# Kernel optimization log

Measured on AMD Instinct MI355X. Metric: run time of the kernel, lower is better.

Reference implementation:

```python
import jax, jax.numpy as jnp
import numpy as np

D_MODEL = 1024
N_HEADS = 16
D_K = 64
BATCH = 2
SEQ = 2048
LN_EPS = 1e-5


def setup_inputs() -> dict:
    key = jax.random.key(0)
    ks = jax.random.split(key, 6)
    s = 1.0 / np.sqrt(D_MODEL)
    return {
        "h": jax.random.normal(ks[0], (BATCH, SEQ, D_MODEL), dtype=jnp.float32),
        "Wq": jax.random.normal(ks[1], (D_MODEL, D_MODEL), dtype=jnp.float32) * s,
        "bq": jnp.zeros((D_MODEL,), jnp.float32),
        "Wk": jax.random.normal(ks[2], (D_MODEL, D_MODEL), dtype=jnp.float32) * s,
        "bk": jnp.zeros((D_MODEL,), jnp.float32),
        "Wv": jax.random.normal(ks[3], (D_MODEL, D_MODEL), dtype=jnp.float32) * s,
        "bv": jnp.zeros((D_MODEL,), jnp.float32),
        "Wo": jax.random.normal(ks[4], (D_MODEL, D_MODEL), dtype=jnp.float32) * s,
        "bo": jnp.zeros((D_MODEL,), jnp.float32),
        "ln_w": jnp.ones((D_MODEL,), jnp.float32),
        "ln_b": jnp.zeros((D_MODEL,), jnp.float32),
    }


def _layernorm(x, w, b):
    mu = jnp.mean(x, axis=-1, keepdims=True)
    var = jnp.var(x, axis=-1, keepdims=True)
    return (x - mu) * jax.lax.rsqrt(var + LN_EPS) * w + b


def reference(h, Wq, bq, Wk, bk, Wv, bv, Wo, bo, ln_w, ln_b):
    b, s, _ = h.shape
    scale = 1.0 / np.sqrt(D_K)
    h_res = h
    hn = _layernorm(h, ln_w, ln_b)
    # Linear layers (torch convention: y = x @ W.T + b), split into heads
    q = (hn @ Wq.T + bq).reshape(b, s, N_HEADS, D_K)
    k = (hn @ Wk.T + bk).reshape(b, s, N_HEADS, D_K)
    v = (hn @ Wv.T + bv).reshape(b, s, N_HEADS, D_K)
    attn = jnp.einsum('bihd,bjhd->bhij', q, k) * scale  # [b, h, i, j]
    attn = jax.nn.softmax(attn, axis=-1)
    o = jnp.einsum('bhij,bjhd->bihd', attn, v).reshape(b, s, N_HEADS * D_K)
    out = o @ Wo.T + bo
    return out + h_res
```

## Files before the change

kernel.cpp:

```cpp
#include <hip/hip_runtime.h>
#include <cstdint>

#define D_MODEL 1024
#define N_HEADS 16
#define D_K     64
#define BATCH   2
#define SEQ     2048
#define TOKENS  (BATCH * SEQ)
#define LN_EPS  1e-5f
#define QSCALE  0.18033688011112042f

typedef __bf16 bf16x8 __attribute__((ext_vector_type(8)));
typedef float  floatx4 __attribute__((ext_vector_type(4)));

__device__ __forceinline__ unsigned short f2bf(float f) {
  union { float f; unsigned u; } v; v.f = f;
  unsigned r = v.u + 0x7fffu + ((v.u >> 16) & 1u);
  return (unsigned short)(r >> 16);
}
__device__ __forceinline__ unsigned pk2bf(float hi, float lo) {
  union { float f; unsigned u; } a, b;
  a.f = hi; b.f = lo;
  return __builtin_amdgcn_perm(a.u, b.u, 0x07060302u);
}

__device__ __forceinline__ void cp16(void* lds, const void* g) {
  __builtin_amdgcn_global_load_lds(
      (__attribute__((address_space(1))) void*)g,
      (__attribute__((address_space(3))) void*)lds, 16, 0, 0);
}

__global__ __launch_bounds__(256) void prep_kernel(
    const float* __restrict__ h, const float* __restrict__ w0,
    const float* __restrict__ w1, const float* __restrict__ w2,
    const float* __restrict__ w3, const float* __restrict__ lw,
    const float* __restrict__ lb, unsigned short* __restrict__ Wcat,
    unsigned short* __restrict__ hn) {
  if (blockIdx.x < 4096) {
    int wsel = blockIdx.x >> 10;
    const float* s = (wsel == 0) ? w0 : (wsel == 1) ? w1 : (wsel == 2) ? w2 : w3;
    unsigned short* d = Wcat + ((size_t)wsel << 20);
    int i = ((blockIdx.x & 1023) << 8) + threadIdx.x;
    float4 v = reinterpret_cast<const float4*>(s)[i];
    ushort4 o;
    o.x = f2bf(v.x); o.y = f2bf(v.y); o.z = f2bf(v.z); o.w = f2bf(v.w);
    reinterpret_cast<ushort4*>(d)[i] = o;
    return;
  }
  int row = blockIdx.x - 4096;
  const float* x = h + (size_t)row * D_MODEL;
  float4 v = reinterpret_cast<const float4*>(x)[threadIdx.x];
  float s  = v.x + v.y + v.z + v.w;
  float s2 = v.x * v.x + v.y * v.y + v.z * v.z + v.w * v.w;
  for (int m = 1; m < 64; m <<= 1) {
    s  += __shfl_xor(s, m);
    s2 += __shfl_xor(s2, m);
  }
  __shared__ float ls[4], ls2[4];
  int wave = threadIdx.x >> 6;
  if ((threadIdx.x & 63) == 0) { ls[wave] = s; ls2[wave] = s2; }
  __syncthreads();
  s  = ls[0] + ls[1] + ls[2] + ls[3];
  s2 = ls2[0] + ls2[1] + ls2[2] + ls2[3];
  float mu  = s * (1.0f / D_MODEL);
  float var = s2 * (1.0f / D_MODEL) - mu * mu;
  float rs  = rsqrtf(var + LN_EPS);
  float4 wv = reinterpret_cast<const float4*>(lw)[threadIdx.x];
  float4 bv = reinterpret_cast<const float4*>(lb)[threadIdx.x];
  ushort4 o;
  o.x = f2bf((v.x - mu) * rs * wv.x + bv.x);
  o.y = f2bf((v.y - mu) * rs * wv.y + bv.y);
  o.z = f2bf((v.z - mu) * rs * wv.z + bv.z);
  o.w = f2bf((v.w - mu) * rs * wv.w + bv.w);
  reinterpret_cast<ushort4*>(hn + (size_t)row * D_MODEL)[threadIdx.x] = o;
}

__global__ __launch_bounds__(256) void gemm_qkv_kernel(
    const unsigned short* __restrict__ A, const unsigned short* __restrict__ Wcat,
    const float* __restrict__ bq, const float* __restrict__ bk,
    const float* __restrict__ bv,
    unsigned short* __restrict__ QK, unsigned short* __restrict__ VtG) {
  __shared__ unsigned short As[128 * 64];
  __shared__ unsigned short Bs[128 * 64];

  const int tid  = threadIdx.x;
  const int w    = tid >> 6;
  const int lane = tid & 63;
  const int l15  = lane & 15;
  const int quad = lane >> 4;
  const int sw   = l15 & 7;
  const int wm = (w >> 1) * 64;
  const int wn = (w & 1) * 64;
  const int bm = blockIdx.y * 128;
  const int bn = blockIdx.x * 128;

  const int srow = tid >> 3;
  const int swzc = (((tid & 7) ^ (srow & 7)) * 8);
  const unsigned short* ga = A    + (size_t)(bm + srow) * 1024 + swzc;
  const unsigned short* gb = Wcat + (size_t)(bn + srow) * 1024 + swzc;
  unsigned short* asl = As + w * 512;
  unsigned short* bsl = Bs + w * 512;

  floatx4 acc[4][4];
  for (int i = 0; i < 4; ++i)
    for (int j = 0; j < 4; ++j) acc[i][j] = {0.f, 0.f, 0.f, 0.f};

  for (int k0 = 0; k0 < 1024; k0 += 64) {
#pragma unroll
    for (int i = 0; i < 4; ++i) cp16(asl + i * 2048, ga + (size_t)i * 32 * 1024 + k0);
#pragma unroll
    for (int i = 0; i < 4; ++i) cp16(bsl + i * 2048, gb + (size_t)i * 32 * 1024 + k0);
    __syncthreads();
#pragma unroll
    for (int kb = 0; kb < 2; ++kb) {
      bf16x8 af[4], bfr[4];
#pragma unroll
      for (int mi = 0; mi < 4; ++mi)
        af[mi] = *reinterpret_cast<const bf16x8*>(
            As + (wm + mi * 16 + l15) * 64 + (((kb * 4 + quad) ^ sw) * 8));
#pragma unroll
      for (int ni = 0; ni < 4; ++ni)
        bfr[ni] = *reinterpret_cast<const bf16x8*>(
            Bs + (wn + ni * 16 + l15) * 64 + (((kb * 4 + quad) ^ sw) * 8));
#pragma unroll
      for (int mi = 0; mi < 4; ++mi)
#pragma unroll
        for (int ni = 0; ni < 4; ++ni)
          acc[mi][ni] = __builtin_amdgcn_mfma_f32_16x16x32_bf16(af[mi], bfr[ni], acc[mi][ni], 0, 0, 0);
    }
    __syncthreads();
  }

  const int wsel = blockIdx.x >> 3;
  if (wsel == 0) {
#pragma unroll
    for (int mi = 0; mi < 4; ++mi)
#pragma unroll
      for (int ni = 0; ni < 4; ++ni) {
        int col = bn + wn + ni * 16 + l15;
        float bb = bq[col];
#pragma unroll
        for (int r = 0; r < 4; ++r) {
          int row = bm + wm + mi * 16 + quad * 4 + r;
          QK[(size_t)row * 2048 + col] = f2bf((acc[mi][ni][r] + bb) * QSCALE);
        }
      }
  } else if (wsel == 1) {
#pragma unroll
    for (int mi = 0; mi < 4; ++mi)
#pragma unroll
      for (int ni = 0; ni < 4; ++ni) {
        int col = bn + wn + ni * 16 + l15;
        float bb = bk[col - 1024];
#pragma unroll
        for (int r = 0; r < 4; ++r) {
          int row = bm + wm + mi * 16 + quad * 4 + r;
          QK[(size_t)row * 2048 + col] = f2bf(acc[mi][ni][r] + bb);
        }
      }
  } else {
#pragma unroll
    for (int mi = 0; mi < 4; ++mi)
#pragma unroll
      for (int ni = 0; ni < 4; ++ni) {
        int d = bn + wn + ni * 16 + l15 - 2048;
        float bb = bv[d];
        ushort4 o;
        o.x = f2bf(acc[mi][ni][0] + bb);
        o.y = f2bf(acc[mi][ni][1] + bb);
        o.z = f2bf(acc[mi][ni][2] + bb);
        o.w = f2bf(acc[mi][ni][3] + bb);
        int row0 = bm + wm + mi * 16 + quad * 4;
        *reinterpret_cast<ushort4*>(VtG + (size_t)d * 4096 + row0) = o;
      }
  }
}

__global__ __launch_bounds__(256) void gemm_out_kernel(
    const unsigned short* __restrict__ A, const unsigned short* __restrict__ Bt,
    const float* __restrict__ bo, const float* __restrict__ resid,
    float* __restrict__ out) {
  __shared__ unsigned short As[128 * 64];
  __shared__ unsigned short Bs[64 * 64];

  const int tid  = threadIdx.x;
  const int w    = tid >> 6;
  const int lane = tid & 63;
  const int l15  = lane & 15;
  const int quad = lane >> 4;
  const int sw   = l15 & 7;
  const int wm = (w >> 1) * 64;
  const int wn = (w & 1) * 32;
  const int bm = blockIdx.y * 128;
  const int bn = blockIdx.x * 64;

  const int srow = tid >> 3;
  const int swzc = (((tid & 7) ^ (srow & 7)) * 8);
  const unsigned short* ga = A  + (size_t)(bm + srow) * 1024 + swzc;
  const unsigned short* gb = Bt + (size_t)(bn + srow) * 1024 + swzc;
  unsigned short* asl = As + w * 512;
  unsigned short* bsl = Bs + w * 512;

  floatx4 acc[4][2];
  for (int i = 0; i < 4; ++i)
    for (int j = 0; j < 2; ++j) acc[i][j] = {0.f, 0.f, 0.f, 0.f};

  for (int k0 = 0; k0 < 1024; k0 += 64) {
#pragma unroll
    for (int i = 0; i < 4; ++i) cp16(asl + i * 2048, ga + (size_t)i * 32 * 1024 + k0);
#pragma unroll
    for (int i = 0; i < 2; ++i) cp16(bsl + i * 2048, gb + (size_t)i * 32 * 1024 + k0);
    __syncthreads();
#pragma unroll
    for (int kb = 0; kb < 2; ++kb) {
      bf16x8 af[4], bfr[2];
#pragma unroll
      for (int mi = 0; mi < 4; ++mi)
        af[mi] = *reinterpret_cast<const bf16x8*>(
            As + (wm + mi * 16 + l15) * 64 + (((kb * 4 + quad) ^ sw) * 8));
#pragma unroll
      for (int ni = 0; ni < 2; ++ni)
        bfr[ni] = *reinterpret_cast<const bf16x8*>(
            Bs + (wn + ni * 16 + l15) * 64 + (((kb * 4 + quad) ^ sw) * 8));
#pragma unroll
      for (int mi = 0; mi < 4; ++mi)
#pragma unroll
        for (int ni = 0; ni < 2; ++ni)
          acc[mi][ni] = __builtin_amdgcn_mfma_f32_16x16x32_bf16(af[mi], bfr[ni], acc[mi][ni], 0, 0, 0);
    }
    __syncthreads();
  }

#pragma unroll
  for (int mi = 0; mi < 4; ++mi)
#pragma unroll
    for (int ni = 0; ni < 2; ++ni) {
      int col = bn + wn + ni * 16 + l15;
      float bb = bo[col];
#pragma unroll
      for (int r = 0; r < 4; ++r) {
        int row = bm + wm + mi * 16 + quad * 4 + r;
        size_t idx = (size_t)row * 1024 + col;
        out[idx] = acc[mi][ni][r] + bb + resid[idx];
      }
    }
}

__global__ __launch_bounds__(256) void attn_kernel(
    const unsigned short* __restrict__ QK, const unsigned short* __restrict__ VtG,
    unsigned short* __restrict__ O) {
  __shared__ unsigned short Ks[2][128 * 64];
  __shared__ unsigned short Vs[2][64 * 128];
  __shared__ unsigned short Pl[4][32 * 64];

  const int tid  = threadIdx.x;
  const int w    = tid >> 6;
  const int lane = tid & 63;
  const int l15  = lane & 15;
  const int quad = lane >> 4;
  const int sw   = l15 & 7;

  const int hh = blockIdx.x, qt = blockIdx.y, bz = blockIdx.z;
  const int tq0  = bz * SEQ + qt * 128;
  const int hoff = hh * 64;

  bf16x8 qf[2][2];
#pragma unroll
  for (int ms = 0; ms < 2; ++ms) {
    const unsigned short* qp =
        QK + (size_t)(tq0 + w * 32 + ms * 16 + l15) * 2048 + hoff;
    qf[ms][0] = *reinterpret_cast<const bf16x8*>(qp + quad * 8);
    qf[ms][1] = *reinterpret_cast<const bf16x8*>(qp + 32 + quad * 8);
  }

  bf16x8 ones;
#pragma unroll
  for (int j = 0; j < 8; ++j) ones[j] = (__bf16)1.0f;

  floatx4 oacc[2][4], lacc[2];
#pragma unroll
  for (int ms = 0; ms < 2; ++ms) {
    lacc[ms] = {0.f, 0.f, 0.f, 0.f};
#pragma unroll
    for (int d = 0; d < 4; ++d) oacc[ms][d] = {0.f, 0.f, 0.f, 0.f};
  }

  const unsigned short* kg = QK + 1024 + hoff
      + (size_t)(bz * SEQ + (tid >> 3)) * 2048
      + (((tid & 7) ^ ((tid >> 3) & 7)) * 8);
  const unsigned short* vg = VtG
      + (size_t)(hoff + (tid >> 4)) * 4096 + bz * SEQ
      + (((tid & 15) ^ ((tid >> 4) & 7)) * 8);
  unsigned short* wp = Pl[w];

  auto stage = [&](int kt, int b) {
    const unsigned short* kgi = kg + (size_t)(kt * 128) * 2048;
    const unsigned short* vgi = vg + kt * 128;
    unsigned short* ksl = Ks[b] + w * 512;
    unsigned short* vsl = Vs[b] + w * 512;
#pragma unroll
    for (int i = 0; i < 4; ++i) cp16(ksl + i * 2048, kgi + (size_t)(i * 32) * 2048);
#pragma unroll
    for (int i = 0; i < 4; ++i) cp16(vsl + i * 2048, vgi + (size_t)(i * 16) * 4096);
  };

  stage(0, 0);

  for (int kt = 0; kt < SEQ / 128; ++kt) {
    __syncthreads();
    if (kt + 1 < SEQ / 128) stage(kt + 1, (kt + 1) & 1);
    const unsigned short* Kb = Ks[kt & 1];
    const unsigned short* Vb = Vs[kt & 1];

    floatx4 ss[2][8];
#pragma unroll
    for (int ms = 0; ms < 2; ++ms)
#pragma unroll
      for (int nb = 0; nb < 8; ++nb) ss[ms][nb] = {0.f, 0.f, 0.f, 0.f};
#pragma unroll
    for (int nb = 0; nb < 8; ++nb) {
      const unsigned short* krow = Kb + (nb * 16 + l15) * 64;
      bf16x8 kf0 = *reinterpret_cast<const bf16x8*>(krow + ((quad ^ sw) * 8));
      bf16x8 kf1 = *reinterpret_cast<const bf16x8*>(krow + (((4 + quad) ^ sw) * 8));
#pragma unroll
      for (int ms = 0; ms < 2; ++ms) {
        ss[ms][nb] = __builtin_amdgcn_mfma_f32_16x16x32_bf16(kf0, qf[ms][0], ss[ms][nb], 0, 0, 0);
        ss[ms][nb] = __builtin_amdgcn_mfma_f32_16x16x32_bf16(kf1, qf[ms][1], ss[ms][nb], 0, 0, 0);
      }
    }

#pragma unroll
    for (int c = 0; c < 2; ++c) {
#pragma unroll
      for (int ms = 0; ms < 2; ++ms)
#pragma unroll
        for (int nb2 = 0; nb2 < 4; ++nb2) {
          floatx4 sv = ss[ms][c * 4 + nb2];
          uint2 pk;
          pk.x = pk2bf(__builtin_amdgcn_exp2f(sv[1]), __builtin_amdgcn_exp2f(sv[0]));
          pk.y = pk2bf(__builtin_amdgcn_exp2f(sv[3]), __builtin_amdgcn_exp2f(sv[2]));
          int rr = ms * 16 + l15;
          int g8 = (nb2 * 2 + (quad >> 1)) ^ sw;
          *reinterpret_cast<uint2*>(wp + rr * 64 + g8 * 8 + (quad & 1) * 4) = pk;
        }
#pragma unroll
      for (int kf = 0; kf < 2; ++kf) {
        bf16x8 pf[2];
#pragma unroll
        for (int ms = 0; ms < 2; ++ms) {
          int rr = ms * 16 + l15;
          int phys = (kf * 4 + quad) ^ sw;
          pf[ms] = *reinterpret_cast<const bf16x8*>(wp + rr * 64 + phys * 8);
          lacc[ms] = __builtin_amdgcn_mfma_f32_16x16x32_bf16(ones, pf[ms], lacc[ms], 0, 0, 0);
        }
#pragma unroll
        for (int db = 0; db < 4; ++db) {
          bf16x8 vf = *reinterpret_cast<const bf16x8*>(
              Vb + (db * 16 + l15) * 128 + ((((c * 2 + kf) * 4 + quad) ^ sw) * 8));
#pragma unroll
          for (int ms = 0; ms < 2; ++ms)
            oacc[ms][db] = __builtin_amdgcn_mfma_f32_16x16x32_bf16(vf, pf[ms], oacc[ms][db], 0, 0, 0);
        }
      }
    }
  }

#pragma unroll
  for (int ms = 0; ms < 2; ++ms) {
    float inv = 1.0f / lacc[ms][0];
    unsigned short* ob = O + (size_t)(tq0 + w * 32 + ms * 16 + l15) * 1024
                       + hoff + quad * 4;
#pragma unroll
    for (int db = 0; db < 4; ++db) {
      uint2 ov;
      ov.x = pk2bf(oacc[ms][db][1] * inv, oacc[ms][db][0] * inv);
      ov.y = pk2bf(oacc[ms][db][3] * inv, oacc[ms][db][2] * inv);
      *reinterpret_cast<uint2*>(ob + db * 16) = ov;
    }
  }
}

extern "C" void kernel_launch(void* const* d_in, const int* in_sizes, int n_in,
                              void* d_out, int out_size, void* d_ws, size_t ws_size,
                              hipStream_t stream) {
  const float* h    = (const float*)d_in[0];
  const float* Wq   = (const float*)d_in[1];
  const float* bq   = (const float*)d_in[2];
  const float* Wk   = (const float*)d_in[3];
  const float* bk   = (const float*)d_in[4];
  const float* Wv   = (const float*)d_in[5];
  const float* bv   = (const float*)d_in[6];
  const float* Wo   = (const float*)d_in[7];
  const float* bo   = (const float*)d_in[8];
  const float* ln_w = (const float*)d_in[9];
  const float* ln_b = (const float*)d_in[10];
  float* out = (float*)d_out;

  unsigned short* ws = (unsigned short*)d_ws;
  const size_t WSZ = (size_t)1 << 20;
  unsigned short* Wcat = ws;
  unsigned short* hn   = Wcat + 4 * WSZ;
  unsigned short* QKb  = hn + (size_t)TOKENS * D_MODEL;
  unsigned short* VtG  = QKb + (size_t)TOKENS * 2048;
  unsigned short* Obuf = VtG + (size_t)D_MODEL * TOKENS;

  prep_kernel<<<8192, 256, 0, stream>>>(h, Wq, Wk, Wv, Wo, ln_w, ln_b, Wcat, hn);

  gemm_qkv_kernel<<<dim3(24, 32), 256, 0, stream>>>(hn, Wcat, bq, bk, bv, QKb, VtG);

  attn_kernel<<<dim3(N_HEADS, SEQ / 128, BATCH), 256, 0, stream>>>(QKb, VtG, Obuf);

  gemm_out_kernel<<<dim3(16, 32), 256, 0, stream>>>(Obuf, Wcat + 3 * WSZ, bo, h, out);
}
```

Measured before the change: 202.0 us.

## Switch attention to 32x32x16 MFMA with register-resident P via lane shuffles

Rewrites the attention inner loop to use 32x32x16 bf16 MFMA tiles instead of 16x16x32. The probability tile is now passed from the score accumulator layout into the PV operand layout through cross-half lane shuffles, so the per-wave LDS round trip for P goes away. The row sum is computed with scalar adds and a shuffle instead of a ones-vector MFMA. This cuts LDS traffic and the extra MFMAs, at the cost of shuffle instructions and larger accumulator register use.

```diff
diff --git a/kernel.cpp b/kernel.cpp
--- a/kernel.cpp
+++ b/kernel.cpp
@@ -11,7 +11,8 @@
 #define QSCALE  0.18033688011112042f
 
 typedef __bf16 bf16x8 __attribute__((ext_vector_type(8)));
-typedef float  floatx4 __attribute__((ext_vector_type(4)));
+typedef float  floatx4  __attribute__((ext_vector_type(4)));
+typedef float  floatx16 __attribute__((ext_vector_type(16)));
 
 __device__ __forceinline__ unsigned short f2bf(float f) {
   union { float f; unsigned u; } v; v.f = f;
@@ -251,39 +252,33 @@
     unsigned short* __restrict__ O) {
   __shared__ unsigned short Ks[2][128 * 64];
   __shared__ unsigned short Vs[2][64 * 128];
-  __shared__ unsigned short Pl[4][32 * 64];
 
   const int tid  = threadIdx.x;
   const int w    = tid >> 6;
   const int lane = tid & 63;
-  const int l15  = lane & 15;
-  const int quad = lane >> 4;
-  const int sw   = l15 & 7;
+  const int l31  = lane & 31;
+  const int h    = lane >> 5;
+  const int s7   = l31 & 7;
 
   const int hh = blockIdx.x, qt = blockIdx.y, bz = blockIdx.z;
   const int tq0  = bz * SEQ + qt * 128;
   const int hoff = hh * 64;
 
-  bf16x8 qf[2][2];
-#pragma unroll
-  for (int ms = 0; ms < 2; ++ms) {
+  bf16x8 qf[4];
+  {
     const unsigned short* qp =
-        QK + (size_t)(tq0 + w * 32 + ms * 16 + l15) * 2048 + hoff;
-    qf[ms][0] = *reinterpret_cast<const bf16x8*>(qp + quad * 8);
-    qf[ms][1] = *reinterpret_cast<const bf16x8*>(qp + 32 + quad * 8);
-  }
-
-  bf16x8 ones;
-#pragma unroll
-  for (int j = 0; j < 8; ++j) ones[j] = (__bf16)1.0f;
-
-  floatx4 oacc[2][4], lacc[2];
-#pragma unroll
-  for (int ms = 0; ms < 2; ++ms) {
-    lacc[ms] = {0.f, 0.f, 0.f, 0.f};
-#pragma unroll
-    for (int d = 0; d < 4; ++d) oacc[ms][d] = {0.f, 0.f, 0.f, 0.f};
-  }
+        QK + (size_t)(tq0 + w * 32 + l31) * 2048 + hoff + h * 8;
+#pragma unroll
+    for (int kd = 0; kd < 4; ++kd)
+      qf[kd] = *reinterpret_cast<const bf16x8*>(qp + kd * 16);
+  }
+
+  floatx16 oacc[2];
+#pragma unroll
+  for (int db = 0; db < 2; ++db)
+#pragma unroll
+    for (int r = 0; r < 16; ++r) oacc[db][r] = 0.f;
+  float lsum = 0.f;
 
   const unsigned short* kg = QK + 1024 + hoff
       + (size_t)(bz * SEQ + (tid >> 3)) * 2048
@@ -291,7 +286,6 @@
   const unsigned short* vg = VtG
       + (size_t)(hoff + (tid >> 4)) * 4096 + bz * SEQ
       + (((tid & 15) ^ ((tid >> 4) & 7)) * 8);
-  unsigned short* wp = Pl[w];
 
   auto stage = [&](int kt, int b) {
     const unsigned short* kgi = kg + (size_t)(kt * 128) * 2048;
@@ -312,72 +306,70 @@
     const unsigned short* Kb = Ks[kt & 1];
     const unsigned short* Vb = Vs[kt & 1];
 
-    floatx4 ss[2][8];
-#pragma unroll
-    for (int ms = 0; ms < 2; ++ms)
-#pragma unroll
-      for (int nb = 0; nb < 8; ++nb) ss[ms][nb] = {0.f, 0.f, 0.f, 0.f};
-#pragma unroll
-    for (int nb = 0; nb < 8; ++nb) {
-      const unsigned short* krow = Kb + (nb * 16 + l15) * 64;
-      bf16x8 kf0 = *reinterpret_cast<const bf16x8*>(krow + ((quad ^ sw) * 8));
-      bf16x8 kf1 = *reinterpret_cast<const bf16x8*>(krow + (((4 + quad) ^ sw) * 8));
-#pragma unroll
-      for (int ms = 0; ms < 2; ++ms) {
-        ss[ms][nb] = __builtin_amdgcn_mfma_f32_16x16x32_bf16(kf0, qf[ms][0], ss[ms][nb], 0, 0, 0);
-        ss[ms][nb] = __builtin_amdgcn_mfma_f32_16x16x32_bf16(kf1, qf[ms][1], ss[ms][nb], 0, 0, 0);
-      }
-    }
-
-#pragma unroll
-    for (int c = 0; c < 2; ++c) {
-#pragma unroll
-      for (int ms = 0; ms < 2; ++ms)
-#pragma unroll
-        for (int nb2 = 0; nb2 < 4; ++nb2) {
-          floatx4 sv = ss[ms][c * 4 + nb2];
-          uint2 pk;
-          pk.x = pk2bf(__builtin_amdgcn_exp2f(sv[1]), __builtin_amdgcn_exp2f(sv[0]));
-          pk.y = pk2bf(__builtin_amdgcn_exp2f(sv[3]), __builtin_amdgcn_exp2f(sv[2]));
-          int rr = ms * 16 + l15;
-          int g8 = (nb2 * 2 + (quad >> 1)) ^ sw;
-          *reinterpret_cast<uint2*>(wp + rr * 64 + g8 * 8 + (quad & 1) * 4) = pk;
+    floatx16 ss[4];
+#pragma unroll
+    for (int kb = 0; kb < 4; ++kb)
+#pragma unroll
+      for (int r = 0; r < 16; ++r) ss[kb][r] = 0.f;
+#pragma unroll
+    for (int kb = 0; kb < 4; ++kb) {
+      const unsigned short* krow = Kb + (kb * 32 + l31) * 64;
+#pragma unroll
+      for (int kd = 0; kd < 4; ++kd) {
+        bf16x8 kf = *reinterpret_cast<const bf16x8*>(
+            krow + (((kd * 2 + h) ^ s7) * 8));
+        ss[kb] = __builtin_amdgcn_mfma_f32_32x32x16_bf16(kf, qf[kd], ss[kb], 0, 0, 0);
+      }
+    }
+
+#pragma unroll
+    for (int kb = 0; kb < 4; ++kb) {
+      float e[16];
+      float bs = 0.f;
+#pragma unroll
+      for (int r = 0; r < 16; ++r) {
+        e[r] = __builtin_amdgcn_exp2f(ss[kb][r]);
+        bs += e[r];
+      }
+      bs += __shfl_xor(bs, 32);
+      lsum += bs;
+      unsigned p[8];
+#pragma unroll
+      for (int i = 0; i < 8; ++i) p[i] = pk2bf(e[2 * i + 1], e[2 * i]);
+
+#pragma unroll
+      for (int sub = 0; sub < 2; ++sub) {
+        unsigned pl0 = p[sub * 4 + 0], pl1 = p[sub * 4 + 1];
+        unsigned ph0 = p[sub * 4 + 2], ph1 = p[sub * 4 + 3];
+        unsigned rec0 = __shfl_xor((int)(h ? pl0 : ph0), 32);
+        unsigned rec1 = __shfl_xor((int)(h ? pl1 : ph1), 32);
+        union { unsigned u[4]; bf16x8 v; } pf;
+        pf.u[0] = h ? rec0 : pl0;
+        pf.u[1] = h ? rec1 : pl1;
+        pf.u[2] = h ? ph0 : rec0;
+        pf.u[3] = h ? ph1 : rec1;
+#pragma unroll
+        for (int db = 0; db < 2; ++db) {
+          bf16x8 vf = *reinterpret_cast<const bf16x8*>(
+              Vb + (db * 32 + l31) * 128 + (((kb * 4 + sub * 2 + h) ^ s7) * 8));
+          oacc[db] = __builtin_amdgcn_mfma_f32_32x32x16_bf16(vf, pf.v, oacc[db], 0, 0, 0);
         }
-#pragma unroll
-      for (int kf = 0; kf < 2; ++kf) {
-        bf16x8 pf[2];
-#pragma unroll
-        for (int ms = 0; ms < 2; ++ms) {
-          int rr = ms * 16 + l15;
-          int phys = (kf * 4 + quad) ^ sw;
-          pf[ms] = *reinterpret_cast<const bf16x8*>(wp + rr * 64 + phys * 8);
-          lacc[ms] = __builtin_amdgcn_mfma_f32_16x16x32_bf16(ones, pf[ms], lacc[ms], 0, 0, 0);
-        }
-#pragma unroll
-        for (int db = 0; db < 4; ++db) {
-          bf16x8 vf = *reinterpret_cast<const bf16x8*>(
-              Vb + (db * 16 + l15) * 128 + ((((c * 2 + kf) * 4 + quad) ^ sw) * 8));
-#pragma unroll
-          for (int ms = 0; ms < 2; ++ms)
-            oacc[ms][db] = __builtin_amdgcn_mfma_f32_16x16x32_bf16(vf, pf[ms], oacc[ms][db], 0, 0, 0);
-        }
-      }
-    }
-  }
-
-#pragma unroll
-  for (int ms = 0; ms < 2; ++ms) {
-    float inv = 1.0f / lacc[ms][0];
-    unsigned short* ob = O + (size_t)(tq0 + w * 32 + ms * 16 + l15) * 1024
-                       + hoff + quad * 4;
-#pragma unroll
-    for (int db = 0; db < 4; ++db) {
+      }
+    }
+  }
+
+  float inv = 1.0f / lsum;
+  unsigned short* ob = O + (size_t)(tq0 + w * 32 + l31) * 1024 + hoff;
+#pragma unroll
+  for (int db = 0; db < 2; ++db)
+#pragma unroll
+    for (int rg = 0; rg < 4; ++rg) {
+      int d0 = db * 32 + rg * 8 + h * 4;
       uint2 ov;
-      ov.x = pk2bf(oacc[ms][db][1] * inv, oacc[ms][db][0] * inv);
-      ov.y = pk2bf(oacc[ms][db][3] * inv, oacc[ms][db][2] * inv);
-      *reinterpret_cast<uint2*>(ob + db * 16) = ov;
-    }
-  }
+      ov.x = pk2bf(oacc[db][rg * 4 + 1] * inv, oacc[db][rg * 4 + 0] * inv);
+      ov.y = pk2bf(oacc[db][rg * 4 + 3] * inv, oacc[db][rg * 4 + 2] * inv);
+      *reinterpret_cast<uint2*>(ob + d0) = ov;
+    }
 }
 
 extern "C" void kernel_launch(void* const* d_in, const int* in_sizes, int n_in,
```

Result: no change. 201.9 us (-0.1%).
